# Kernel optimization log

Measured on AMD Instinct MI355X. Metric: run time of the kernel, lower is better.

The kernel has to match this reference:

```python
import jax, jax.numpy as jnp
import numpy as np

NC, NF = 64, 16
Z_NEAR, Z_FAR = 2.0, 6.0
EPS = 1e-5


def volume_integral(z_vals, sigmas, radiances):
    # z_vals/sigmas: (B,R,Z,1), radiances: (B,R,Z,F)
    d = z_vals[..., 1:, :] - z_vals[..., :-1, :]
    dists = jnp.concatenate([d, d[..., -1:, :]], axis=-2)            # (B,R,Z,1)
    alpha = 1.0 - jnp.exp(-jax.nn.relu(sigmas) * dists)
    alpha_shifted = jnp.concatenate(
        [jnp.ones_like(alpha[..., :1, :]), 1.0 - alpha + 1e-10], axis=-2)
    Ts = jnp.cumprod(alpha_shifted, axis=-2)                         # transmittance
    weights = alpha * Ts[..., :-1, :]                                # (B,R,Z,1)
    rgb = jnp.sum(weights * radiances, axis=-2)                      # (B,R,F)
    depth = jnp.sum(weights * z_vals, axis=-2)                       # (B,R,1)
    return rgb, depth, weights


def sample_pdf(bins, weights, u, eps=EPS):
    # bins: (N, S+1), weights: (N, S), u: (N, Nf) in [0,1)
    weights = weights + eps
    pdf = weights / jnp.sum(weights, -1, keepdims=True)
    cdf = jnp.cumsum(pdf, -1)
    cdf = jnp.concatenate([jnp.zeros_like(cdf[:, :1]), cdf], -1)     # (N, S+1)
    inds = jax.vmap(jnp.searchsorted)(cdf, u)                        # side='left' == torch default
    below = jnp.clip(inds - 1, 0, None)
    above = jnp.minimum(inds, weights.shape[-1])
    cdf_g0 = jnp.take_along_axis(cdf, below, 1)
    cdf_g1 = jnp.take_along_axis(cdf, above, 1)
    bins_g0 = jnp.take_along_axis(bins, below, 1)
    bins_g1 = jnp.take_along_axis(bins, above, 1)
    denom = cdf_g1 - cdf_g0
    denom = jnp.where(denom < eps, 1.0, denom)
    return bins_g0 + (u - cdf_g0) / denom * (bins_g1 - bins_g0)


def _render(ros, rds, w_sigma, w_feat, u):
    B, R, _ = ros.shape

    def rad(pts):
        return pts @ w_sigma, jax.nn.sigmoid(pts @ w_feat)

    # coarse stratified samples (lindisp=False)
    zl = jnp.linspace(0.0, 1.0, NC, dtype=ros.dtype)
    z_vals = Z_NEAR + (Z_FAR - Z_NEAR) * zl                          # (NC,)
    z_vals = jnp.broadcast_to(z_vals[None, None, :, None], (B, R, NC, 1))
    pts = ros[:, :, None, :] + rds[:, :, None, :] * z_vals           # (B,R,NC,3)
    sigma, feats = rad(pts)

    # coarse pass + importance resampling (no grad in original)
    _, _, weights = volume_integral(z_vals, sigma, feats)
    weights = jax.lax.stop_gradient(weights).reshape(B * R, NC)
    t = z_vals.reshape(B * R, NC)
    tm = 0.5 * (t[:, :-1] + t[:, 1:])                                # (N, NC-1)
    t_pdf = sample_pdf(tm, weights[:, 1:-1], u)                      # (N, NF)
    t_pdf = jax.lax.stop_gradient(t_pdf).reshape(B, R, NF)

    pts_fine = ros[:, :, None, :] + rds[:, :, None, :] * t_pdf[..., None]
    pts_all = jnp.concatenate([pts, pts_fine], axis=-2)              # (B,R,NC+NF,3)
    sigma_all, feats_all = rad(pts_all)

    # merge-sort coarse+fine by depth and gather
    z_all = jnp.concatenate([z_vals, t_pdf[..., None]], axis=-2)     # (B,R,Z,1)
    idx = jnp.argsort(z_all, axis=-2)
    z_all = jnp.take_along_axis(z_all, idx, axis=-2)
    sigma_all = jnp.take_along_axis(sigma_all, idx, axis=-2)
    feats_all = jnp.take_along_axis(
        feats_all, jnp.broadcast_to(idx, feats_all.shape), axis=-2)

    rgb, depth, weights = volume_integral(z_all, sigma_all, feats_all)
    return rgb, depth, weights


def setup_inputs() -> dict:
    key = jax.random.key(0)
    k = jax.random.split(key, 5)
    B, R = 8, 16384
    return {
        "ros": jax.random.normal(k[0], (B, R, 3), jnp.float32),
        "rds": jax.random.normal(k[1], (B, R, 3), jnp.float32),
        "w_sigma": jax.random.normal(k[2], (3, 1), jnp.float32),
        "w_feat": jax.random.normal(k[3], (3, 3), jnp.float32),
        "u": jax.random.uniform(k[4], (B * R, NF), jnp.float32),
    }


def reference(ros, rds, w_sigma, w_feat, u):
    return _render(ros, rds, w_sigma, w_feat, u)
```

## Files before the change

kernel.cpp:

```cpp
#include <hip/hip_runtime.h>

#define NCC 64
#define NFF 16
#define NZ  80
#define BLK 128
#define STRIDE 97

__device__ __forceinline__ float zc_of(int i) {
    return fmaf(4.0f, (float)i * (1.0f / 63.0f), 2.0f);
}
__device__ __forceinline__ float tm_of(int i) {
    return 0.5f * (zc_of(i) + zc_of(i + 1));
}
__device__ __forceinline__ float fast_rcp(float x) { return __builtin_amdgcn_rcpf(x); }
__device__ __forceinline__ float sigmoidf(float x) { return fast_rcp(1.0f + __expf(-x)); }

__global__ void __launch_bounds__(BLK, 2)
VolumeRenderer_16192026706363_kernel(const float* __restrict__ ros,
                                     const float* __restrict__ rds,
                                     const float* __restrict__ w_sigma,
                                     const float* __restrict__ w_feat,
                                     const float* __restrict__ u,
                                     float* __restrict__ out,
                                     int nrays)
{
    __shared__ float lds[BLK * STRIDE];
    const int tid = threadIdx.x;
    const int n = blockIdx.x * BLK + tid;
    float* my = &lds[tid * STRIDE];

    const float ro0 = ros[n * 3 + 0], ro1 = ros[n * 3 + 1], ro2 = ros[n * 3 + 2];
    const float rd0 = rds[n * 3 + 0], rd1 = rds[n * 3 + 1], rd2 = rds[n * 3 + 2];
    const float s0 = w_sigma[0], s1 = w_sigma[1], s2 = w_sigma[2];
    float wf[9];
#pragma unroll
    for (int k = 0; k < 9; k++) wf[k] = w_feat[k];

    float T = 1.0f, cum = 0.0f;
    float dist = zc_of(1) - zc_of(0);
    my[0] = 0.0f;
    for (int i = 0; i < NCC; i++) {
        float z = zc_of(i);
        if (i < NCC - 1) dist = zc_of(i + 1) - z;
        float p0 = fmaf(rd0, z, ro0);
        float p1 = fmaf(rd1, z, ro1);
        float p2 = fmaf(rd2, z, ro2);
        float sg = p0 * s0 + p1 * s1 + p2 * s2;
        float e = __expf(-fmaxf(sg, 0.0f) * dist);
        float alpha = 1.0f - e;
        float w = alpha * T;
        T *= (1.0f - alpha + 1e-10f);
        if (i >= 1 && i <= 62) {
            cum += w + 1e-5f;
            my[i] = cum;
        }
    }
    const float invS = 1.0f / cum;
    for (int i = 1; i <= 62; i++) my[i] *= invS;

    const float4* u4p = reinterpret_cast<const float4*>(u + (size_t)n * 16);
    float tv[16];
#pragma unroll
    for (int q = 0; q < 4; q++) {
        float4 uq = u4p[q];
#pragma unroll
        for (int r = 0; r < 4; r++) {
            float uu;
            if (r == 0) uu = uq.x; else if (r == 1) uu = uq.y;
            else if (r == 2) uu = uq.z; else uu = uq.w;
            int lo = 0, hi = 63;
#pragma unroll
            for (int s = 0; s < 6; s++) {
                int mid = (lo + hi) >> 1;
                bool lt = (my[mid] < uu);
                lo = lt ? mid + 1 : lo;
                hi = lt ? hi : mid;
            }
            int ind = lo;
            int below = (ind - 1 > 0) ? ind - 1 : 0;
            int above = (ind < 62) ? ind : 62;
            float c0 = my[below], c1 = my[above];
            float b0 = tm_of(below), b1 = tm_of(above);
            float denom = c1 - c0;
            denom = (denom < 1e-5f) ? 1.0f : denom;
            tv[q * 4 + r] = fmaf((uu - c0) / denom, (b1 - b0), b0);
        }
    }

#pragma unroll
    for (int k = 2; k <= 16; k <<= 1) {
#pragma unroll
        for (int j = k >> 1; j > 0; j >>= 1) {
#pragma unroll
            for (int i = 0; i < 16; i++) {
                int l = i ^ j;
                if (l > i) {
                    float a = tv[i], b = tv[l];
                    float mn = fminf(a, b), mx = fmaxf(a, b);
                    bool up = ((i & k) == 0);
                    tv[i] = up ? mn : mx;
                    tv[l] = up ? mx : mn;
                }
            }
        }
    }
#pragma unroll
    for (int i = 0; i < 16; i++) my[80 + i] = tv[i];

    int ic = 0, jf = 0;
    float zch = 2.0f;
    float zfh = my[80];
    float T2 = 1.0f, acc0 = 0.0f, acc1 = 0.0f, acc2 = 0.0f, accd = 0.0f;

    auto pop = [&]() -> float {
        float r;
        bool takeC = (zch <= zfh);
        if (takeC) {
            r = zch; ic++;
            zch = (ic < NCC) ? zc_of(ic) : 3.0e38f;
        } else {
            r = zfh; jf++;
            zfh = (jf < NFF) ? my[80 + jf] : 3.0e38f;
        }
        return r;
    };

    auto process = [&](float z, float d, int slot) {
        float p0 = fmaf(rd0, z, ro0);
        float p1 = fmaf(rd1, z, ro1);
        float p2 = fmaf(rd2, z, ro2);
        float sg = p0 * s0 + p1 * s1 + p2 * s2;
        float e = __expf(-fmaxf(sg, 0.0f) * d);
        float alpha = 1.0f - e;
        float w = alpha * T2;
        T2 *= (1.0f - alpha + 1e-10f);
        my[slot] = w;
        float f0 = sigmoidf(fmaf(p0, wf[0], fmaf(p1, wf[3], p2 * wf[6])));
        float f1 = sigmoidf(fmaf(p0, wf[1], fmaf(p1, wf[4], p2 * wf[7])));
        float f2 = sigmoidf(fmaf(p0, wf[2], fmaf(p1, wf[5], p2 * wf[8])));
        acc0 = fmaf(w, f0, acc0);
        acc1 = fmaf(w, f1, acc1);
        acc2 = fmaf(w, f2, acc2);
        accd = fmaf(w, z, accd);
    };

    float zprev = pop();
    float dlast = 0.0f;
    for (int i = 1; i < NZ; i++) {
        float z = pop();
        float d = z - zprev;
        process(zprev, d, i - 1);
        zprev = z; dlast = d;
    }
    process(zprev, dlast, NZ - 1);

    out[(size_t)n * 3 + 0] = acc0;
    out[(size_t)n * 3 + 1] = acc1;
    out[(size_t)n * 3 + 2] = acc2;
    out[(size_t)nrays * 3 + n] = accd;

    __syncthreads();
    const size_t wbase = (size_t)nrays * 4 + (size_t)blockIdx.x * BLK * NZ;
    for (int k = tid; k < BLK * NZ; k += BLK) {
        int t = k / NZ;
        int i = k - t * NZ;
        out[wbase + k] = lds[t * STRIDE + i];
    }
}

extern "C" void kernel_launch(void* const* d_in, const int* in_sizes, int n_in,
                              void* d_out, int out_size, void* d_ws, size_t ws_size,
                              hipStream_t stream) {
    const float* ros = (const float*)d_in[0];
    const float* rds = (const float*)d_in[1];
    const float* w_sigma = (const float*)d_in[2];
    const float* w_feat = (const float*)d_in[3];
    const float* u = (const float*)d_in[4];
    float* out = (float*)d_out;

    int nrays = in_sizes[0] / 3;
    int grid = nrays / BLK;
    VolumeRenderer_16192026706363_kernel<<<grid, BLK, 0, stream>>>(
        ros, rds, w_sigma, w_feat, u, out, nrays);
}
```

Measured before the change: 127.4 us.

## Write weights directly as float4, shrink LDS, precompute linear sigma/feature terms

Drops the LDS-staged coalesced write of the 80 per-ray weights and instead has each thread store its weights straight to global memory as float4 chunks. This removes the 97-float LDS stride and the block barrier, shrinking LDS to 63 floats per thread, which can raise occupancy. Sigma and feature projections are precomputed as affine functions of z, exp2 is used in place of exp, and the CDF normalization is deferred by scaling the search key. The trade-off is that weight stores are now strided across threads (320 bytes apart) rather than coalesced.

New measurement: 107.6 us. 1.18x faster.

```diff
diff --git a/kernel.cpp b/kernel.cpp
--- a/kernel.cpp
+++ b/kernel.cpp
@@ -4,7 +4,7 @@
 #define NFF 16
 #define NZ  80
 #define BLK 128
-#define STRIDE 97
+#define SLOTS 63
 
 __device__ __forceinline__ float zc_of(int i) {
     return fmaf(4.0f, (float)i * (1.0f / 63.0f), 2.0f);
@@ -13,7 +13,6 @@
     return 0.5f * (zc_of(i) + zc_of(i + 1));
 }
 __device__ __forceinline__ float fast_rcp(float x) { return __builtin_amdgcn_rcpf(x); }
-__device__ __forceinline__ float sigmoidf(float x) { return fast_rcp(1.0f + __expf(-x)); }
 
 __global__ void __launch_bounds__(BLK, 2)
 VolumeRenderer_16192026706363_kernel(const float* __restrict__ ros,
@@ -24,67 +23,74 @@
                                      float* __restrict__ out,
                                      int nrays)
 {
-    __shared__ float lds[BLK * STRIDE];
+    __shared__ float lds[BLK * SLOTS];
     const int tid = threadIdx.x;
     const int n = blockIdx.x * BLK + tid;
-    float* my = &lds[tid * STRIDE];
+    float* my = &lds[tid * SLOTS];
+
+    const float4* u4p = reinterpret_cast<const float4*>(u + (size_t)n * 16);
+    float4 uq0 = u4p[0], uq1 = u4p[1], uq2 = u4p[2], uq3 = u4p[3];
 
     const float ro0 = ros[n * 3 + 0], ro1 = ros[n * 3 + 1], ro2 = ros[n * 3 + 2];
     const float rd0 = rds[n * 3 + 0], rd1 = rds[n * 3 + 1], rd2 = rds[n * 3 + 2];
     const float s0 = w_sigma[0], s1 = w_sigma[1], s2 = w_sigma[2];
-    float wf[9];
+    const float sgA = ro0 * s0 + ro1 * s1 + ro2 * s2;
+    const float sgB = rd0 * s0 + rd1 * s1 + rd2 * s2;
+    float fA[3], fB[3];
 #pragma unroll
-    for (int k = 0; k < 9; k++) wf[k] = w_feat[k];
+    for (int c = 0; c < 3; c++) {
+        fA[c] = ro0 * w_feat[0 * 3 + c] + ro1 * w_feat[1 * 3 + c] + ro2 * w_feat[2 * 3 + c];
+        fB[c] = rd0 * w_feat[0 * 3 + c] + rd1 * w_feat[1 * 3 + c] + rd2 * w_feat[2 * 3 + c];
+    }
+
+    const float LOG2E = 1.4426950408889634f;
+    const float DIST  = 4.0f / 63.0f;
+    const float K1    = -DIST * LOG2E;
 
     float T = 1.0f, cum = 0.0f;
-    float dist = zc_of(1) - zc_of(0);
     my[0] = 0.0f;
-    for (int i = 0; i < NCC; i++) {
-        float z = zc_of(i);
-        if (i < NCC - 1) dist = zc_of(i + 1) - z;
-        float p0 = fmaf(rd0, z, ro0);
-        float p1 = fmaf(rd1, z, ro1);
-        float p2 = fmaf(rd2, z, ro2);
-        float sg = p0 * s0 + p1 * s1 + p2 * s2;
-        float e = __expf(-fmaxf(sg, 0.0f) * dist);
-        float alpha = 1.0f - e;
-        float w = alpha * T;
-        T *= (1.0f - alpha + 1e-10f);
-        if (i >= 1 && i <= 62) {
-            cum += w + 1e-5f;
-            my[i] = cum;
-        }
+    {
+        float e = exp2f(fmaxf(sgA + sgB * 2.0f, 0.0f) * K1);
+        T = e + 1e-10f;
     }
-    const float invS = 1.0f / cum;
-    for (int i = 1; i <= 62; i++) my[i] *= invS;
+    for (int i = 1; i <= 62; i++) {
+        float sg = fmaf(sgB, zc_of(i), sgA);
+        float e = exp2f(fmaxf(sg, 0.0f) * K1);
+        float w = (1.0f - e) * T;
+        cum += w + 1e-5f;
+        my[i] = cum;
+        T *= (e + 1e-10f);
+    }
+    const float S = cum;
+    const float invS = 1.0f / S;
 
-    const float4* u4p = reinterpret_cast<const float4*>(u + (size_t)n * 16);
     float tv[16];
 #pragma unroll
-    for (int q = 0; q < 4; q++) {
-        float4 uq = u4p[q];
+    for (int q = 0; q < 16; q++) {
+        float uu;
+        {
+            float4 uq = (q < 4) ? uq0 : (q < 8) ? uq1 : (q < 12) ? uq2 : uq3;
+            int r = q & 3;
+            uu = (r == 0) ? uq.x : (r == 1) ? uq.y : (r == 2) ? uq.z : uq.w;
+        }
+        float us = uu * S;
+        int lo = 0, hi = 63;
 #pragma unroll
-        for (int r = 0; r < 4; r++) {
-            float uu;
-            if (r == 0) uu = uq.x; else if (r == 1) uu = uq.y;
-            else if (r == 2) uu = uq.z; else uu = uq.w;
-            int lo = 0, hi = 63;
-#pragma unroll
-            for (int s = 0; s < 6; s++) {
-                int mid = (lo + hi) >> 1;
-                bool lt = (my[mid] < uu);
-                lo = lt ? mid + 1 : lo;
-                hi = lt ? hi : mid;
-            }
-            int ind = lo;
-            int below = (ind - 1 > 0) ? ind - 1 : 0;
-            int above = (ind < 62) ? ind : 62;
-            float c0 = my[below], c1 = my[above];
-            float b0 = tm_of(below), b1 = tm_of(above);
-            float denom = c1 - c0;
-            denom = (denom < 1e-5f) ? 1.0f : denom;
-            tv[q * 4 + r] = fmaf((uu - c0) / denom, (b1 - b0), b0);
+        for (int s = 0; s < 6; s++) {
+            int mid = (lo + hi) >> 1;
+            bool lt = (my[mid] < us);
+            lo = lt ? mid + 1 : lo;
+            hi = lt ? hi : mid;
         }
+        int ind = lo;
+        int below = (ind - 1 > 0) ? ind - 1 : 0;
+        int above = (ind < 62) ? ind : 62;
+        float c0 = my[below] * invS, c1 = my[above] * invS;
+        float b0 = tm_of(below);
+        float denom = c1 - c0;
+        denom = (denom < 1e-5f) ? 1.0f : denom;
+        float db = (4.0f / 63.0f) * (float)(above - below);
+        tv[q] = fmaf((uu - c0) / denom, db, b0);
     }
 
 #pragma unroll
@@ -105,67 +111,67 @@
         }
     }
 #pragma unroll
-    for (int i = 0; i < 16; i++) my[80 + i] = tv[i];
+    for (int i = 0; i < 16; i++) my[i] = tv[i];
 
     int ic = 0, jf = 0;
     float zch = 2.0f;
-    float zfh = my[80];
+    float zfh = my[0];
     float T2 = 1.0f, acc0 = 0.0f, acc1 = 0.0f, acc2 = 0.0f, accd = 0.0f;
 
     auto pop = [&]() -> float {
-        float r;
         bool takeC = (zch <= zfh);
-        if (takeC) {
-            r = zch; ic++;
-            zch = (ic < NCC) ? zc_of(ic) : 3.0e38f;
-        } else {
-            r = zfh; jf++;
-            zfh = (jf < NFF) ? my[80 + jf] : 3.0e38f;
-        }
+        float r = takeC ? zch : zfh;
+        if (takeC) { ic++; zch = (ic < NCC) ? zc_of(ic) : 3.0e38f; }
+        else       { jf++; zfh = (jf < NFF) ? my[jf] : 3.0e38f; }
         return r;
     };
 
-    auto process = [&](float z, float d, int slot) {
-        float p0 = fmaf(rd0, z, ro0);
-        float p1 = fmaf(rd1, z, ro1);
-        float p2 = fmaf(rd2, z, ro2);
-        float sg = p0 * s0 + p1 * s1 + p2 * s2;
-        float e = __expf(-fmaxf(sg, 0.0f) * d);
+    auto proc = [&](float z, float d) -> float {
+        float sg = fmaf(sgB, z, sgA);
+        float e = exp2f(fmaxf(sg, 0.0f) * d * (-LOG2E));
         float alpha = 1.0f - e;
         float w = alpha * T2;
-        T2 *= (1.0f - alpha + 1e-10f);
-        my[slot] = w;
-        float f0 = sigmoidf(fmaf(p0, wf[0], fmaf(p1, wf[3], p2 * wf[6])));
-        float f1 = sigmoidf(fmaf(p0, wf[1], fmaf(p1, wf[4], p2 * wf[7])));
-        float f2 = sigmoidf(fmaf(p0, wf[2], fmaf(p1, wf[5], p2 * wf[8])));
+        T2 *= (e + 1e-10f);
+        float f0 = fast_rcp(1.0f + exp2f(fmaf(fB[0], z, fA[0]) * (-LOG2E)));
+        float f1 = fast_rcp(1.0f + exp2f(fmaf(fB[1], z, fA[1]) * (-LOG2E)));
+        float f2 = fast_rcp(1.0f + exp2f(fmaf(fB[2], z, fA[2]) * (-LOG2E)));
         acc0 = fmaf(w, f0, acc0);
         acc1 = fmaf(w, f1, acc1);
         acc2 = fmaf(w, f2, acc2);
         accd = fmaf(w, z, accd);
+        return w;
     };
 
+    float* wptr = out + (size_t)nrays * 4 + (size_t)n * NZ;
     float zprev = pop();
     float dlast = 0.0f;
-    for (int i = 1; i < NZ; i++) {
+    float wq[4];
+
+    for (int g = 0; g < 19; g++) {
+#pragma unroll
+        for (int j = 0; j < 4; j++) {
+            float z = pop();
+            wq[j] = proc(zprev, z - zprev);
+            zprev = z;
+        }
+        *reinterpret_cast<float4*>(wptr + g * 4) =
+            make_float4(wq[0], wq[1], wq[2], wq[3]);
+    }
+#pragma unroll
+    for (int j = 0; j < 3; j++) {
         float z = pop();
-        float d = z - zprev;
-        process(zprev, d, i - 1);
-        zprev = z; dlast = d;
+        dlast = z - zprev;
+        wq[j] = proc(zprev, dlast);
+        zprev = z;
     }
-    process(zprev, dlast, NZ - 1);
+    wq[3] = proc(zprev, dlast);
+    *reinterpret_cast<float4*>(wptr + 19 * 4) =
+        make_float4(wq[0], wq[1], wq[2], wq[3]);
 
     out[(size_t)n * 3 + 0] = acc0;
     out[(size_t)n * 3 + 1] = acc1;
     out[(size_t)n * 3 + 2] = acc2;
     out[(size_t)nrays * 3 + n] = accd;
-
-    __syncthreads();
-    const size_t wbase = (size_t)nrays * 4 + (size_t)blockIdx.x * BLK * NZ;
-    for (int k = tid; k < BLK * NZ; k += BLK) {
-        int t = k / NZ;
-        int i = k - t * NZ;
-        out[wbase + k] = lds[t * STRIDE + i];
-    }
 }
 
 extern "C" void kernel_launch(void* const* d_in, const int* in_sizes, int n_in,
```
